# Optimization experiments

Measured on AMD Instinct MI355X. Metric: run time of the kernel, lower is better.

The kernel has to match this reference:

```python
import jax, jax.numpy as jnp
import numpy as np

S, B, D, NH = 4096, 4, 1024, 16


def _unitnorm(v):
    # v / ||v||_2 along last dim (matches torch.norm(v, dim=-1))
    return v / jnp.linalg.norm(v, axis=-1, keepdims=True)


def setup_inputs() -> dict:
    key = jax.random.key(0)
    ks = jax.random.split(key, 9)
    scale = 1.0 / np.sqrt(D)
    inp = {
        "h": jax.random.normal(ks[0], (S, B, D), dtype=jnp.float32),
        "Wq_w": jax.random.normal(ks[1], (D, D), dtype=jnp.float32) * scale,
        "Wq_b": jax.random.normal(ks[2], (D,), dtype=jnp.float32) * scale,
        "Wk_w": jax.random.normal(ks[3], (D, D), dtype=jnp.float32) * scale,
        "Wk_b": jax.random.normal(ks[4], (D,), dtype=jnp.float32) * scale,
        "Wv_w": jax.random.normal(ks[5], (D, D), dtype=jnp.float32) * scale,
        "Wv_b": jax.random.normal(ks[6], (D,), dtype=jnp.float32) * scale,
        "Wo_w": jax.random.normal(ks[7], (D, D), dtype=jnp.float32) * scale,
        "Wo_b": jax.random.normal(ks[8], (D,), dtype=jnp.float32) * scale,
        "nhead": NH,
    }
    return inp


def reference(h, Wq_w, Wq_b, Wk_w, Wk_b, Wv_w, Wv_b, Wo_w, Wo_b, nhead):
    s, b, d = h.shape
    dh = d // nhead

    def proj(W, bias):
        # torch nn.Linear: x @ W.T + b, then split heads -> [S,B,NH,dh]
        return (h @ W.T + bias).reshape(s, b, nhead, dh)

    k = jax.nn.elu(_unitnorm(proj(Wk_w, Wk_b)))  # unitelu
    v = proj(Wv_w, Wv_b)
    q = _unitnorm(proj(Wq_w, Wq_b))  # sigma = unitnorm (default)

    # Linear-attention state: sum of outer products over the whole sequence
    A = jnp.einsum('sbnq,sbnv->bnvq', k, v)  # [B,NH,dh,dh]
    out = jnp.einsum('sbnq,bnvq->sbnv', q, A).reshape(s, b, d)
    out = out @ Wo_w.T + Wo_b
    return out, k, q
```

## Files before the change

### kernel.cpp

```cpp
#include <hip/hip_runtime.h>
#include <hip/hip_bf16.h>
#include <math.h>

#define S_LEN 4096
#define B_SZ  4
#define D_DIM 1024
#define NHEAD 16
#define R_ROWS (S_LEN * B_SZ)

#define AS1 __attribute__((address_space(1)))
#define AS3 __attribute__((address_space(3)))

typedef __bf16 bf16_t;
typedef __attribute__((ext_vector_type(8))) __bf16 bf16x8;
typedef __attribute__((ext_vector_type(4))) __bf16 bf16x4;
typedef __attribute__((ext_vector_type(4))) float  f32x4;

#define MFMA16 __builtin_amdgcn_mfma_f32_16x16x32_bf16

__device__ __forceinline__ void gload16(const bf16_t* g, bf16_t* l) {
  __builtin_amdgcn_global_load_lds((const AS1 unsigned int*)g,
                                   (AS3 unsigned int*)l, 16, 0, 0);
}
__device__ __forceinline__ void hard_barrier() {
  asm volatile("s_barrier" ::: "memory");
}

__global__ void k_cvt(const float* __restrict__ src, bf16_t* __restrict__ dst, int n) {
  int i = (blockIdx.x * 256 + threadIdx.x) * 4;
  if (i >= n) return;
  f32x4 v = *(const f32x4*)(src + i);
  bf16x4 o;
  o[0] = (bf16_t)v[0]; o[1] = (bf16_t)v[1]; o[2] = (bf16_t)v[2]; o[3] = (bf16_t)v[3];
  *(bf16x4*)(dst + i) = o;
}

__device__ __forceinline__ void gemm_core_256(
    const bf16_t* __restrict__ A, const bf16_t* __restrict__ B,
    int row0, int col0,
    bf16_t (&sA)[3][8192], bf16_t (&sB)[3][8192], f32x4 (&acc)[8][4])
{
  const int tid  = threadIdx.x;
  const int wave = tid >> 6, lane = tid & 63;
  const int lr = lane & 15, lg = lane >> 4;
  const int wr = wave >> 2, wn = wave & 3;
  const int grow = tid >> 2;
  const int gch  = (tid & 3) ^ (grow & 3);

  auto stageA = [&](int buf, int k0, int j) {
    gload16(&A[(size_t)(row0 + j * 128 + grow) * D_DIM + k0 + gch * 8],
            &sA[buf][(j * 512 + wave * 64) * 8]);
  };
  auto stageB = [&](int buf, int k0, int j) {
    gload16(&B[(size_t)(col0 + j * 128 + grow) * D_DIM + k0 + gch * 8],
            &sB[buf][(j * 512 + wave * 64) * 8]);
  };

  int aoff[8], boff[4];
  #pragma unroll
  for (int m = 0; m < 8; m++) {
    const int r = wr * 128 + m * 16 + lr;
    aoff[m] = r * 32 + (lg ^ (r & 3)) * 8;
  }
  #pragma unroll
  for (int n = 0; n < 4; n++) {
    const int r = wn * 64 + n * 16 + lr;
    boff[n] = r * 32 + (lg ^ (r & 3)) * 8;
  }

  #pragma unroll
  for (int m = 0; m < 8; m++)
    #pragma unroll
    for (int n = 0; n < 4; n++)
      #pragma unroll
      for (int r = 0; r < 4; r++) acc[m][n][r] = 0.f;

  stageA(0, 0, 0); stageA(0, 0, 1); stageB(0, 0, 0); stageB(0, 0, 1);
  stageA(1, 32, 0); stageA(1, 32, 1); stageB(1, 32, 0); stageB(1, 32, 1);
  asm volatile("s_waitcnt vmcnt(4)" ::: "memory");
  hard_barrier();

  for (int t = 0; t < 32; ++t) {
    const int c  = t % 3;
    const int cn = (t + 2) % 3;
    const int kn = (t + 2) * 32;
    const bool st = (t < 30);

    bf16x8 bfr[4], afr[4];
    #pragma unroll
    for (int n = 0; n < 4; ++n) bfr[n] = *(const bf16x8*)&sB[c][boff[n]];
    #pragma unroll
    for (int m = 0; m < 4; ++m) afr[m] = *(const bf16x8*)&sA[c][aoff[m]];
    if (st) { stageA(cn, kn, 0); stageA(cn, kn, 1); }
    hard_barrier();
    asm volatile("s_waitcnt lgkmcnt(0)" ::: "memory");
    __builtin_amdgcn_sched_barrier(0);
    __builtin_amdgcn_s_setprio(1);
    #pragma unroll
    for (int m = 0; m < 4; ++m)
      #pragma unroll
      for (int n = 0; n < 4; ++n)
        acc[m][n] = MFMA16(afr[m], bfr[n], acc[m][n], 0, 0, 0);
    __builtin_amdgcn_s_setprio(0);
    hard_barrier();

    #pragma unroll
    for (int m = 0; m < 4; ++m) afr[m] = *(const bf16x8*)&sA[c][aoff[m + 4]];
    if (st) { stageB(cn, kn, 0); stageB(cn, kn, 1); }
    hard_barrier();
    asm volatile("s_waitcnt lgkmcnt(0)" ::: "memory");
    __builtin_amdgcn_sched_barrier(0);
    __builtin_amdgcn_s_setprio(1);
    #pragma unroll
    for (int m = 0; m < 4; ++m)
      #pragma unroll
      for (int n = 0; n < 4; ++n)
        acc[m + 4][n] = MFMA16(afr[m], bfr[n], acc[m + 4][n], 0, 0, 0);
    __builtin_amdgcn_s_setprio(0);
    if (t < 30)       asm volatile("s_waitcnt vmcnt(4)" ::: "memory");
    else if (t == 30) asm volatile("s_waitcnt vmcnt(0)" ::: "memory");
    hard_barrier();
  }
}

__global__ __launch_bounds__(512, 2) void k_proj(
    const bf16_t* __restrict__ hB, const bf16_t* __restrict__ Wcat,
    const float* __restrict__ bq, const float* __restrict__ bk, const float* __restrict__ bv,
    bf16_t* __restrict__ outVb, float* __restrict__ outK, float* __restrict__ outQ,
    bf16_t* __restrict__ qBm)
{
  __shared__ bf16_t sA[3][8192];
  __shared__ bf16_t sB[3][8192];

  const int tid  = threadIdx.x;
  const int wave = tid >> 6, lane = tid & 63;
  const int lr = lane & 15, lg = lane >> 4;
  const int wr = wave >> 2, wn = wave & 3;
  const int row0 = blockIdx.x * 256;
  const int by   = blockIdx.y;

  f32x4 acc[8][4];
  gemm_core_256(hB, Wcat, row0, by * 256, sA, sB, acc);

  const int sec = by >> 2;
  const int hc0 = (by & 3) * 256 + wn * 64;
  const float* bias = (sec == 0) ? bq : (sec == 1 ? bk : bv);
  float bvv[4];
  #pragma unroll
  for (int n = 0; n < 4; n++) bvv[n] = bias[hc0 + n * 16 + lr];

  #pragma unroll
  for (int m = 0; m < 8; ++m) {
    #pragma unroll
    for (int r = 0; r < 4; ++r) {
      const int gm = row0 + wr * 128 + m * 16 + lg * 4 + r;
      float v[4];
      float ss = 0.f;
      #pragma unroll
      for (int n = 0; n < 4; n++) {
        v[n] = acc[m][n][r] + bvv[n];
        ss += v[n] * v[n];
      }
      if (sec == 2) {
        #pragma unroll
        for (int n = 0; n < 4; n++)
          outVb[(size_t)gm * D_DIM + hc0 + n * 16 + lr] = (bf16_t)v[n];
      } else {
        #pragma unroll
        for (int msk = 1; msk < 16; msk <<= 1) ss += __shfl_xor(ss, msk);
        const float rs = 1.0f / sqrtf(ss);
        if (sec == 0) {
          const size_t qrow = (size_t)(gm & 3) * S_LEN + (gm >> 2);
          #pragma unroll
          for (int n = 0; n < 4; n++) {
            const float qn = v[n] * rs;
            outQ[(size_t)gm * D_DIM + hc0 + n * 16 + lr] = qn;
            qBm[qrow * D_DIM + hc0 + n * 16 + lr] = (bf16_t)qn;
          }
        } else {
          #pragma unroll
          for (int n = 0; n < 4; n++) {
            float kn = v[n] * rs;
            kn = kn > 0.f ? kn : expm1f(kn);
            outK[(size_t)gm * D_DIM + hc0 + n * 16 + lr] = kn;
          }
        }
      }
    }
  }
}

__global__ __launch_bounds__(256) void k_state(
    const float* __restrict__ Kf, const bf16_t* __restrict__ Vb,
    float* __restrict__ Apart)
{
  const int bn = blockIdx.x;
  const int ch = blockIdx.y;
  const int b = bn >> 4, n = bn & 15;
  const int tid = threadIdx.x;
  const int ti = tid >> 4, tj = tid & 15;

  __shared__ float sV[32][64];
  __shared__ float sK[32][64];

  float acc[4][4];
  #pragma unroll
  for (int i = 0; i < 4; i++)
    #pragma unroll
    for (int j = 0; j < 4; j++) acc[i][j] = 0.f;

  const int rr = tid >> 3, cc = (tid & 7) * 8;
  for (int s0 = ch * 512; s0 < ch * 512 + 512; s0 += 32) {
    const size_t g = (size_t)((s0 + rr) * B_SZ + b) * D_DIM + n * 64 + cc;
    bf16x8 v8 = *(const bf16x8*)&Vb[g];
    #pragma unroll
    for (int e = 0; e < 8; e++) sV[rr][cc + e] = (float)v8[e];
    *(f32x4*)&sK[rr][cc]     = *(const f32x4*)&Kf[g];
    *(f32x4*)&sK[rr][cc + 4] = *(const f32x4*)&Kf[g + 4];
    __syncthreads();
    #pragma unroll
    for (int ss = 0; ss < 32; ss++) {
      f32x4 vv = *(const f32x4*)&sV[ss][ti * 4];
      f32x4 kk = *(const f32x4*)&sK[ss][tj * 4];
      #pragma unroll
      for (int i = 0; i < 4; i++)
        #pragma unroll
        for (int j = 0; j < 4; j++)
          acc[i][j] = fmaf(vv[i], kk[j], acc[i][j]);
    }
    __syncthreads();
  }
  float* ap = Apart + ((size_t)ch * 64 + bn) * 4096;
  #pragma unroll
  for (int i = 0; i < 4; i++)
    #pragma unroll
    for (int j = 0; j < 4; j++)
      ap[(ti * 4 + i) * 64 + tj * 4 + j] = acc[i][j];
}

__global__ __launch_bounds__(256) void k_combine(
    const float* __restrict__ Apart, const bf16_t* __restrict__ WoB,
    bf16_t* __restrict__ Ct)
{
  const int bn = blockIdx.x;
  const int dp = blockIdx.y;
  const int b = bn >> 4, n = bn & 15;
  const int tid = threadIdx.x;
  const int ti = tid >> 4, tj = tid & 15;

  __shared__ float sAm[64][65];
  __shared__ float sW[64][65];

  #pragma unroll
  for (int p = 0; p < 16; p++) {
    const int idx = tid + p * 256;
    float s = 0.f;
    #pragma unroll
    for (int c2 = 0; c2 < 8; c2++)
      s += Apart[((size_t)c2 * 64 + bn) * 4096 + idx];
    sAm[idx >> 6][idx & 63] = s;
  }
  {
    const int r = tid >> 2, cv = (tid & 3) * 16;
    bf16x8 w0 = *(const bf16x8*)&WoB[(size_t)(dp * 64 + r) * D_DIM + n * 64 + cv];
    bf16x8 w1 = *(const bf16x8*)&WoB[(size_t)(dp * 64 + r) * D_DIM + n * 64 + cv + 8];
    #pragma unroll
    for (int e = 0; e < 8; e++) {
      sW[r][cv + e]     = (float)w0[e];
      sW[r][cv + 8 + e] = (float)w1[e];
    }
  }
  __syncthreads();

  float acc[4][4];
  #pragma unroll
  for (int i = 0; i < 4; i++)
    #pragma unroll
    for (int j = 0; j < 4; j++) acc[i][j] = 0.f;

  for (int dv = 0; dv < 64; dv++) {
    float w[4], a[4];
    #pragma unroll
    for (int i = 0; i < 4; i++) w[i] = sW[ti * 4 + i][dv];
    #pragma unroll
    for (int j = 0; j < 4; j++) a[j] = sAm[dv][tj * 4 + j];
    #pragma unroll
    for (int i = 0; i < 4; i++)
      #pragma unroll
      for (int j = 0; j < 4; j++)
        acc[i][j] = fmaf(w[i], a[j], acc[i][j]);
  }
  #pragma unroll
  for (int i = 0; i < 4; i++)
    #pragma unroll
    for (int j = 0; j < 4; j++)
      Ct[((size_t)b * D_DIM + dp * 64 + ti * 4 + i) * D_DIM + n * 64 + tj * 4 + j] =
          (bf16_t)acc[i][j];
}

__global__ __launch_bounds__(512, 2) void k_final(
    const bf16_t* __restrict__ qBm, const bf16_t* __restrict__ Ct,
    const float* __restrict__ bo, float* __restrict__ outO)
{
  __shared__ bf16_t sA[3][8192];
  __shared__ bf16_t sB[3][8192];

  const int tid  = threadIdx.x;
  const int wave = tid >> 6, lane = tid & 63;
  const int lr = lane & 15, lg = lane >> 4;
  const int wr = wave >> 2, wn = wave & 3;
  const int b    = blockIdx.z;
  const int row0 = blockIdx.x * 256;
  const int col0 = blockIdx.y * 256;

  f32x4 acc[8][4];
  gemm_core_256(qBm + (size_t)b * S_LEN * D_DIM, Ct + (size_t)b * D_DIM * D_DIM,
                row0, col0, sA, sB, acc);

  #pragma unroll
  for (int m = 0; m < 8; ++m) {
    #pragma unroll
    for (int r = 0; r < 4; ++r) {
      const int gs = row0 + wr * 128 + m * 16 + lg * 4 + r;
      #pragma unroll
      for (int n = 0; n < 4; n++) {
        const int col = col0 + wn * 64 + n * 16 + lr;
        outO[((size_t)gs * B_SZ + b) * D_DIM + col] = acc[m][n][r] + bo[col];
      }
    }
  }
}

extern "C" void kernel_launch(void* const* d_in, const int* in_sizes, int n_in,
                              void* d_out, int out_size, void* d_ws, size_t ws_size,
                              hipStream_t stream) {
  (void)in_sizes; (void)n_in; (void)out_size; (void)ws_size;
  const float* h  = (const float*)d_in[0];
  const float* Wq = (const float*)d_in[1];
  const float* bq = (const float*)d_in[2];
  const float* Wk = (const float*)d_in[3];
  const float* bk = (const float*)d_in[4];
  const float* Wv = (const float*)d_in[5];
  const float* bv = (const float*)d_in[6];
  const float* Wo = (const float*)d_in[7];
  const float* bo = (const float*)d_in[8];

  float* out0 = (float*)d_out;
  float* outK = out0 + (size_t)R_ROWS * D_DIM;
  float* outQ = outK + (size_t)R_ROWS * D_DIM;
  bf16_t* vB  = (bf16_t*)d_out;

  char* ws = (char*)d_ws;
  bf16_t* hB    = (bf16_t*)ws;
  bf16_t* Ct    = (bf16_t*)ws;
  bf16_t* Wcat  = (bf16_t*)(ws + 33554432);
  bf16_t* WoB   = (bf16_t*)(ws + 33554432 + 6291456);
  float*  Apart = (float*)(ws + 41943040);
  bf16_t* qBm   = (bf16_t*)(ws + 50331648);

  const int nH = R_ROWS * D_DIM;
  const int nW = D_DIM * D_DIM;
  k_cvt<<<nH / 1024, 256, 0, stream>>>(h, hB, nH);
  k_cvt<<<nW / 1024, 256, 0, stream>>>(Wq, Wcat, nW);
  k_cvt<<<nW / 1024, 256, 0, stream>>>(Wk, Wcat + nW, nW);
  k_cvt<<<nW / 1024, 256, 0, stream>>>(Wv, Wcat + 2 * nW, nW);
  k_cvt<<<nW / 1024, 256, 0, stream>>>(Wo, WoB, nW);

  k_proj<<<dim3(R_ROWS / 256, 12), 512, 0, stream>>>(hB, Wcat, bq, bk, bv,
                                                     vB, outK, outQ, qBm);
  k_state<<<dim3(64, 8), 256, 0, stream>>>(outK, vB, Apart);
  k_combine<<<dim3(64, 16), 256, 0, stream>>>(Apart, WoB, Ct);
  k_final<<<dim3(S_LEN / 256, D_DIM / 256, B_SZ), 512, 0, stream>>>(qBm, Ct, bo, out0);
}
```

Before: 265.3 us.

## Restructure GEMM mainloop into 8-phase ping-pong schedule with BK=64 tiles

Result: faster. 254.4 us (-4.1%).

```diff
diff --git a/kernel.cpp b/kernel.cpp
--- a/kernel.cpp
+++ b/kernel.cpp
@@ -22,9 +22,26 @@
   __builtin_amdgcn_global_load_lds((const AS1 unsigned int*)g,
                                    (AS3 unsigned int*)l, 16, 0, 0);
 }
-__device__ __forceinline__ void hard_barrier() {
-  asm volatile("s_barrier" ::: "memory");
-}
+
+#define BAR asm volatile("s_barrier" ::: "memory")
+#define LGKM0 do { asm volatile("s_waitcnt lgkmcnt(0)" ::: "memory"); \
+                   __builtin_amdgcn_sched_barrier(0); } while (0)
+
+#define RD_A(dst, ap, mlo) \
+  _Pragma("unroll") for (int mm = 0; mm < 4; ++mm) \
+    _Pragma("unroll") for (int kx = 0; kx < 2; ++kx) \
+      dst[mm][kx] = *(const bf16x8*)&ap[offA[(mlo) + mm][kx]];
+#define RD_B(dst, bp, nlo) \
+  _Pragma("unroll") for (int nn = 0; nn < 2; ++nn) \
+    _Pragma("unroll") for (int kx = 0; kx < 2; ++kx) \
+      dst[nn][kx] = *(const bf16x8*)&bp[offB[(nlo) + nn][kx]];
+#define QUAD(mb, nb, AF, BF) \
+  do { __builtin_amdgcn_s_setprio(1); \
+  _Pragma("unroll") for (int mm = 0; mm < 4; ++mm) \
+    _Pragma("unroll") for (int nn = 0; nn < 2; ++nn) { \
+      acc[(mb)+mm][(nb)+nn] = MFMA16(AF[mm][0], BF[nn][0], acc[(mb)+mm][(nb)+nn], 0, 0, 0); \
+      acc[(mb)+mm][(nb)+nn] = MFMA16(AF[mm][1], BF[nn][1], acc[(mb)+mm][(nb)+nn], 0, 0, 0); } \
+  __builtin_amdgcn_s_setprio(0); } while (0)
 
 __global__ void k_cvt(const float* __restrict__ src, bf16_t* __restrict__ dst, int n) {
   int i = (blockIdx.x * 256 + threadIdx.x) * 4;
@@ -35,38 +52,50 @@
   *(bf16x4*)(dst + i) = o;
 }
 
-__device__ __forceinline__ void gemm_core_256(
+__device__ __forceinline__ void gemm_core_8ph(
     const bf16_t* __restrict__ A, const bf16_t* __restrict__ B,
     int row0, int col0,
-    bf16_t (&sA)[3][8192], bf16_t (&sB)[3][8192], f32x4 (&acc)[8][4])
+    bf16_t (&sA)[2][2][8192], bf16_t (&sB)[2][2][8192], f32x4 (&acc)[8][4])
 {
   const int tid  = threadIdx.x;
   const int wave = tid >> 6, lane = tid & 63;
   const int lr = lane & 15, lg = lane >> 4;
   const int wr = wave >> 2, wn = wave & 3;
-  const int grow = tid >> 2;
-  const int gch  = (tid & 3) ^ (grow & 3);
-
-  auto stageA = [&](int buf, int k0, int j) {
-    gload16(&A[(size_t)(row0 + j * 128 + grow) * D_DIM + k0 + gch * 8],
-            &sA[buf][(j * 512 + wave * 64) * 8]);
+  const int grow = tid >> 3;
+  const int gsw  = (tid & 7) ^ (grow & 7);
+
+  auto stA = [&](int buf, int half, int k0) {
+    #pragma unroll
+    for (int j = 0; j < 2; ++j)
+      gload16(&A[(size_t)(row0 + half * 128 + j * 64 + grow) * D_DIM + k0 + gsw * 8],
+              &sA[buf][half][(j * 64 + wave * 8) * 64]);
   };
-  auto stageB = [&](int buf, int k0, int j) {
-    gload16(&B[(size_t)(col0 + j * 128 + grow) * D_DIM + k0 + gch * 8],
-            &sB[buf][(j * 512 + wave * 64) * 8]);
+  auto stB = [&](int buf, int half, int k0) {
+    #pragma unroll
+    for (int j = 0; j < 2; ++j)
+      gload16(&B[(size_t)(col0 + half * 128 + j * 64 + grow) * D_DIM + k0 + gsw * 8],
+              &sB[buf][half][(j * 64 + wave * 8) * 64]);
   };
 
-  int aoff[8], boff[4];
-  #pragma unroll
-  for (int m = 0; m < 8; m++) {
-    const int r = wr * 128 + m * 16 + lr;
-    aoff[m] = r * 32 + (lg ^ (r & 3)) * 8;
-  }
-  #pragma unroll
-  for (int n = 0; n < 4; n++) {
-    const int r = wn * 64 + n * 16 + lr;
-    boff[n] = r * 32 + (lg ^ (r & 3)) * 8;
-  }
+  int offA[8][2], offB[4][2];
+  #pragma unroll
+  for (int m = 0; m < 8; ++m) {
+    const int r = m * 16 + lr;
+    #pragma unroll
+    for (int kx = 0; kx < 2; ++kx)
+      offA[m][kx] = r * 64 + (((kx << 2) + lg) ^ (r & 7)) * 8;
+  }
+  #pragma unroll
+  for (int n = 0; n < 4; ++n) {
+    const int r = (wn & 1) * 64 + n * 16 + lr;
+    #pragma unroll
+    for (int kx = 0; kx < 2; ++kx)
+      offB[n][kx] = r * 64 + (((kx << 2) + lg) ^ (r & 7)) * 8;
+  }
+  const bf16_t* a0 = &sA[0][wr][0];
+  const bf16_t* a1 = &sA[1][wr][0];
+  const bf16_t* b0 = &sB[0][wn >> 1][0];
+  const bf16_t* b1 = &sB[1][wn >> 1][0];
 
   #pragma unroll
   for (int m = 0; m < 8; m++)
@@ -75,51 +104,43 @@
       #pragma unroll
       for (int r = 0; r < 4; r++) acc[m][n][r] = 0.f;
 
-  stageA(0, 0, 0); stageA(0, 0, 1); stageB(0, 0, 0); stageB(0, 0, 1);
-  stageA(1, 32, 0); stageA(1, 32, 1); stageB(1, 32, 0); stageB(1, 32, 1);
-  asm volatile("s_waitcnt vmcnt(4)" ::: "memory");
-  hard_barrier();
-
-  for (int t = 0; t < 32; ++t) {
-    const int c  = t % 3;
-    const int cn = (t + 2) % 3;
-    const int kn = (t + 2) * 32;
-    const bool st = (t < 30);
-
-    bf16x8 bfr[4], afr[4];
-    #pragma unroll
-    for (int n = 0; n < 4; ++n) bfr[n] = *(const bf16x8*)&sB[c][boff[n]];
-    #pragma unroll
-    for (int m = 0; m < 4; ++m) afr[m] = *(const bf16x8*)&sA[c][aoff[m]];
-    if (st) { stageA(cn, kn, 0); stageA(cn, kn, 1); }
-    hard_barrier();
-    asm volatile("s_waitcnt lgkmcnt(0)" ::: "memory");
-    __builtin_amdgcn_sched_barrier(0);
-    __builtin_amdgcn_s_setprio(1);
-    #pragma unroll
-    for (int m = 0; m < 4; ++m)
-      #pragma unroll
-      for (int n = 0; n < 4; ++n)
-        acc[m][n] = MFMA16(afr[m], bfr[n], acc[m][n], 0, 0, 0);
-    __builtin_amdgcn_s_setprio(0);
-    hard_barrier();
-
-    #pragma unroll
-    for (int m = 0; m < 4; ++m) afr[m] = *(const bf16x8*)&sA[c][aoff[m + 4]];
-    if (st) { stageB(cn, kn, 0); stageB(cn, kn, 1); }
-    hard_barrier();
-    asm volatile("s_waitcnt lgkmcnt(0)" ::: "memory");
-    __builtin_amdgcn_sched_barrier(0);
-    __builtin_amdgcn_s_setprio(1);
-    #pragma unroll
-    for (int m = 0; m < 4; ++m)
-      #pragma unroll
-      for (int n = 0; n < 4; ++n)
-        acc[m + 4][n] = MFMA16(afr[m], bfr[n], acc[m + 4][n], 0, 0, 0);
-    __builtin_amdgcn_s_setprio(0);
-    if (t < 30)       asm volatile("s_waitcnt vmcnt(4)" ::: "memory");
-    else if (t == 30) asm volatile("s_waitcnt vmcnt(0)" ::: "memory");
-    hard_barrier();
+  stA(0, 0, 0);  stA(0, 1, 0);  stB(0, 0, 0);  stB(0, 1, 0);
+  stA(1, 0, 64); stA(1, 1, 64); stB(1, 0, 64); stB(1, 1, 64);
+  asm volatile("s_waitcnt vmcnt(8)" ::: "memory");
+  BAR;
+
+  bf16x8 af03[4][2], af47[4][2], bf01[2][2], bf23[2][2];
+
+  #pragma unroll 1
+  for (int i = 0; i < 8; ++i) {
+    const bool last = (i == 7);
+    const int kn0 = (i + 1) * 128, kn1 = kn0 + 64;
+
+    RD_A(af03, a0, 0); RD_B(bf01, b0, 0);
+    BAR; LGKM0; QUAD(0, 0, af03, bf01); BAR;
+    RD_A(af47, a0, 4);
+    BAR; LGKM0; QUAD(4, 0, af47, bf01); BAR;
+    RD_B(bf23, b0, 2);
+    if (!last) stA(0, 0, kn0);
+    BAR; LGKM0; QUAD(0, 2, af03, bf23); BAR;
+    if (!last) { stA(0, 1, kn0); stB(0, 0, kn0); }
+    BAR; QUAD(4, 2, af47, bf23);
+    if (!last) asm volatile("s_waitcnt vmcnt(6)" ::: "memory");
+    else       asm volatile("s_waitcnt vmcnt(0)" ::: "memory");
+    BAR;
+
+    RD_A(af03, a1, 0); RD_B(bf01, b1, 0);
+    if (!last) stB(0, 1, kn0);
+    BAR; LGKM0; QUAD(0, 0, af03, bf01); BAR;
+    RD_A(af47, a1, 4);
+    BAR; LGKM0; QUAD(4, 0, af47, bf01); BAR;
+    RD_B(bf23, b1, 2);
+    if (!last) stA(1, 0, kn1);
+    BAR; LGKM0; QUAD(0, 2, af03, bf23); BAR;
+    if (!last) { stA(1, 1, kn1); stB(1, 0, kn1); stB(1, 1, kn1); }
+    BAR; QUAD(4, 2, af47, bf23);
+    if (!last) asm volatile("s_waitcnt vmcnt(8)" ::: "memory");
+    BAR;
   }
 }
 
@@ -129,8 +150,8 @@
     bf16_t* __restrict__ outVb, float* __restrict__ outK, float* __restrict__ outQ,
     bf16_t* __restrict__ qBm)
 {
-  __shared__ bf16_t sA[3][8192];
-  __shared__ bf16_t sB[3][8192];
+  __shared__ bf16_t sA[2][2][8192];
+  __shared__ bf16_t sB[2][2][8192];
 
   const int tid  = threadIdx.x;
   const int wave = tid >> 6, lane = tid & 63;
@@ -140,7 +161,7 @@
   const int by   = blockIdx.y;
 
   f32x4 acc[8][4];
-  gemm_core_256(hB, Wcat, row0, by * 256, sA, sB, acc);
+  gemm_core_8ph(hB, Wcat, row0, by * 256, sA, sB, acc);
 
   const int sec = by >> 2;
   const int hc0 = (by & 3) * 256 + wn * 64;
@@ -302,8 +323,8 @@
     const bf16_t* __restrict__ qBm, const bf16_t* __restrict__ Ct,
     const float* __restrict__ bo, float* __restrict__ outO)
 {
-  __shared__ bf16_t sA[3][8192];
-  __shared__ bf16_t sB[3][8192];
+  __shared__ bf16_t sA[2][2][8192];
+  __shared__ bf16_t sB[2][2][8192];
 
   const int tid  = threadIdx.x;
   const int wave = tid >> 6, lane = tid & 63;
@@ -314,7 +335,7 @@
   const int col0 = blockIdx.y * 256;
 
   f32x4 acc[8][4];
-  gemm_core_256(qBm + (size_t)b * S_LEN * D_DIM, Ct + (size_t)b * D_DIM * D_DIM,
+  gemm_core_8ph(qBm + (size_t)b * S_LEN * D_DIM, Ct + (size_t)b * D_DIM * D_DIM,
                 row0, col0, sA, sB, acc);
 
   #pragma unroll
```

## Shrink GEMM tiles to 128x128 for higher occupancy and fuse weight conversions

Applied to the files above, without the earlier changes.

After: 270.6 us. Within noise of the previous version (+2.0%).

```diff
diff --git a/kernel.cpp b/kernel.cpp
--- a/kernel.cpp
+++ b/kernel.cpp
@@ -22,9 +22,10 @@
   __builtin_amdgcn_global_load_lds((const AS1 unsigned int*)g,
                                    (AS3 unsigned int*)l, 16, 0, 0);
 }
-__device__ __forceinline__ void hard_barrier() {
-  asm volatile("s_barrier" ::: "memory");
-}
+
+#define BAR asm volatile("s_barrier" ::: "memory")
+#define LGKM0 do { asm volatile("s_waitcnt lgkmcnt(0)" ::: "memory"); \
+                   __builtin_amdgcn_sched_barrier(0); } while (0)
 
 __global__ void k_cvt(const float* __restrict__ src, bf16_t* __restrict__ dst, int n) {
   int i = (blockIdx.x * 256 + threadIdx.x) * 4;
@@ -34,126 +35,116 @@
   o[0] = (bf16_t)v[0]; o[1] = (bf16_t)v[1]; o[2] = (bf16_t)v[2]; o[3] = (bf16_t)v[3];
   *(bf16x4*)(dst + i) = o;
 }
-
-__device__ __forceinline__ void gemm_core_256(
+__global__ void k_cvtw(const float* __restrict__ q, const float* __restrict__ k,
+                       const float* __restrict__ v, const float* __restrict__ o,
+                       bf16_t* __restrict__ dst) {
+  const int sec = blockIdx.x >> 10;
+  const int i = ((blockIdx.x & 1023) * 256 + threadIdx.x) * 4;
+  const float* s = (sec == 0) ? q : (sec == 1) ? k : (sec == 2) ? v : o;
+  f32x4 x = *(const f32x4*)(s + i);
+  bf16x4 y;
+  y[0] = (bf16_t)x[0]; y[1] = (bf16_t)x[1]; y[2] = (bf16_t)x[2]; y[3] = (bf16_t)x[3];
+  *(bf16x4*)(dst + (size_t)sec * 1048576 + i) = y;
+}
+
+__device__ __forceinline__ void gemm_core_occ(
     const bf16_t* __restrict__ A, const bf16_t* __restrict__ B,
     int row0, int col0,
-    bf16_t (&sA)[3][8192], bf16_t (&sB)[3][8192], f32x4 (&acc)[8][4])
+    bf16_t (&sA)[3][4096], bf16_t (&sB)[3][4096], f32x4 (&acc)[2][4])
 {
   const int tid  = threadIdx.x;
   const int wave = tid >> 6, lane = tid & 63;
   const int lr = lane & 15, lg = lane >> 4;
-  const int wr = wave >> 2, wn = wave & 3;
-  const int grow = tid >> 2;
-  const int gch  = (tid & 3) ^ (grow & 3);
-
-  auto stageA = [&](int buf, int k0, int j) {
-    gload16(&A[(size_t)(row0 + j * 128 + grow) * D_DIM + k0 + gch * 8],
-            &sA[buf][(j * 512 + wave * 64) * 8]);
+  const int wr = wave >> 1, wn = wave & 1;
+  const int arow = tid >> 2;
+  const int asw  = (tid & 3) ^ ((arow >> 1) & 3);
+
+  auto stA = [&](int buf, int k0) {
+    gload16(&A[(size_t)(row0 + arow) * D_DIM + k0 + asw * 8],
+            &sA[buf][(wave * 64) * 8]);
   };
-  auto stageB = [&](int buf, int k0, int j) {
-    gload16(&B[(size_t)(col0 + j * 128 + grow) * D_DIM + k0 + gch * 8],
-            &sB[buf][(j * 512 + wave * 64) * 8]);
+  auto stB = [&](int buf, int k0) {
+    gload16(&B[(size_t)(col0 + arow) * D_DIM + k0 + asw * 8],
+            &sB[buf][(wave * 64) * 8]);
   };
 
-  int aoff[8], boff[4];
-  #pragma unroll
-  for (int m = 0; m < 8; m++) {
-    const int r = wr * 128 + m * 16 + lr;
-    aoff[m] = r * 32 + (lg ^ (r & 3)) * 8;
-  }
-  #pragma unroll
-  for (int n = 0; n < 4; n++) {
+  int offA[2], offB[4];
+  #pragma unroll
+  for (int m = 0; m < 2; ++m) {
+    const int r = wr * 32 + m * 16 + lr;
+    offA[m] = r * 32 + ((lg ^ ((r >> 1) & 3)) * 8);
+  }
+  #pragma unroll
+  for (int n = 0; n < 4; ++n) {
     const int r = wn * 64 + n * 16 + lr;
-    boff[n] = r * 32 + (lg ^ (r & 3)) * 8;
-  }
-
-  #pragma unroll
-  for (int m = 0; m < 8; m++)
+    offB[n] = r * 32 + ((lg ^ ((r >> 1) & 3)) * 8);
+  }
+
+  #pragma unroll
+  for (int m = 0; m < 2; m++)
     #pragma unroll
     for (int n = 0; n < 4; n++)
       #pragma unroll
       for (int r = 0; r < 4; r++) acc[m][n][r] = 0.f;
 
-  stageA(0, 0, 0); stageA(0, 0, 1); stageB(0, 0, 0); stageB(0, 0, 1);
-  stageA(1, 32, 0); stageA(1, 32, 1); stageB(1, 32, 0); stageB(1, 32, 1);
-  asm volatile("s_waitcnt vmcnt(4)" ::: "memory");
-  hard_barrier();
-
+  stA(0, 0); stB(0, 0); stA(1, 32); stB(1, 32);
+  asm volatile("s_waitcnt vmcnt(2)" ::: "memory");
+  BAR;
+
+  #pragma unroll 1
   for (int t = 0; t < 32; ++t) {
-    const int c  = t % 3;
-    const int cn = (t + 2) % 3;
-    const int kn = (t + 2) * 32;
-    const bool st = (t < 30);
-
-    bf16x8 bfr[4], afr[4];
-    #pragma unroll
-    for (int n = 0; n < 4; ++n) bfr[n] = *(const bf16x8*)&sB[c][boff[n]];
-    #pragma unroll
-    for (int m = 0; m < 4; ++m) afr[m] = *(const bf16x8*)&sA[c][aoff[m]];
-    if (st) { stageA(cn, kn, 0); stageA(cn, kn, 1); }
-    hard_barrier();
-    asm volatile("s_waitcnt lgkmcnt(0)" ::: "memory");
-    __builtin_amdgcn_sched_barrier(0);
+    const int c = t % 3, cn = (t + 2) % 3;
+    bf16x8 af[2], bf[4];
+    #pragma unroll
+    for (int m = 0; m < 2; ++m) af[m] = *(const bf16x8*)&sA[c][offA[m]];
+    #pragma unroll
+    for (int n = 0; n < 4; ++n) bf[n] = *(const bf16x8*)&sB[c][offB[n]];
+    if (t < 30) { stA(cn, (t + 2) * 32); stB(cn, (t + 2) * 32); }
+    LGKM0;
     __builtin_amdgcn_s_setprio(1);
     #pragma unroll
-    for (int m = 0; m < 4; ++m)
+    for (int m = 0; m < 2; ++m)
       #pragma unroll
       for (int n = 0; n < 4; ++n)
-        acc[m][n] = MFMA16(afr[m], bfr[n], acc[m][n], 0, 0, 0);
+        acc[m][n] = MFMA16(af[m], bf[n], acc[m][n], 0, 0, 0);
     __builtin_amdgcn_s_setprio(0);
-    hard_barrier();
-
-    #pragma unroll
-    for (int m = 0; m < 4; ++m) afr[m] = *(const bf16x8*)&sA[c][aoff[m + 4]];
-    if (st) { stageB(cn, kn, 0); stageB(cn, kn, 1); }
-    hard_barrier();
-    asm volatile("s_waitcnt lgkmcnt(0)" ::: "memory");
-    __builtin_amdgcn_sched_barrier(0);
-    __builtin_amdgcn_s_setprio(1);
-    #pragma unroll
-    for (int m = 0; m < 4; ++m)
-      #pragma unroll
-      for (int n = 0; n < 4; ++n)
-        acc[m + 4][n] = MFMA16(afr[m], bfr[n], acc[m + 4][n], 0, 0, 0);
-    __builtin_amdgcn_s_setprio(0);
-    if (t < 30)       asm volatile("s_waitcnt vmcnt(4)" ::: "memory");
+    if (t < 30)       asm volatile("s_waitcnt vmcnt(2)" ::: "memory");
     else if (t == 30) asm volatile("s_waitcnt vmcnt(0)" ::: "memory");
-    hard_barrier();
-  }
-}
-
-__global__ __launch_bounds__(512, 2) void k_proj(
+    BAR;
+  }
+}
+
+__global__ __launch_bounds__(512, 4) void k_proj(
     const bf16_t* __restrict__ hB, const bf16_t* __restrict__ Wcat,
     const float* __restrict__ bq, const float* __restrict__ bk, const float* __restrict__ bv,
     bf16_t* __restrict__ outVb, float* __restrict__ outK, float* __restrict__ outQ,
     bf16_t* __restrict__ qBm)
 {
-  __shared__ bf16_t sA[3][8192];
-  __shared__ bf16_t sB[3][8192];
+  __shared__ bf16_t sA[3][4096];
+  __shared__ bf16_t sB[3][4096];
 
   const int tid  = threadIdx.x;
   const int wave = tid >> 6, lane = tid & 63;
   const int lr = lane & 15, lg = lane >> 4;
-  const int wr = wave >> 2, wn = wave & 3;
-  const int row0 = blockIdx.x * 256;
+  const int wr = wave >> 1, wn = wave & 1;
+  const int row0 = blockIdx.x * 128;
   const int by   = blockIdx.y;
 
-  f32x4 acc[8][4];
-  gemm_core_256(hB, Wcat, row0, by * 256, sA, sB, acc);
-
-  const int sec = by >> 2;
-  const int hc0 = (by & 3) * 256 + wn * 64;
+  f32x4 acc[2][4];
+  gemm_core_occ(hB, Wcat, row0, by * 128, sA, sB, acc);
+
+  const int sec = by >> 3;
+  const int hc0 = (by & 7) * 128 + wn * 64;
   const float* bias = (sec == 0) ? bq : (sec == 1 ? bk : bv);
   float bvv[4];
   #pragma unroll
   for (int n = 0; n < 4; n++) bvv[n] = bias[hc0 + n * 16 + lr];
 
   #pragma unroll
-  for (int m = 0; m < 8; ++m) {
+  for (int m = 0; m < 2; ++m) {
     #pragma unroll
     for (int r = 0; r < 4; ++r) {
-      const int gm = row0 + wr * 128 + m * 16 + lg * 4 + r;
+      const int gm = row0 + wr * 32 + m * 16 + lg * 4 + r;
       float v[4];
       float ss = 0.f;
       #pragma unroll
@@ -298,30 +289,30 @@
           (bf16_t)acc[i][j];
 }
 
-__global__ __launch_bounds__(512, 2) void k_final(
+__global__ __launch_bounds__(512, 4) void k_final(
     const bf16_t* __restrict__ qBm, const bf16_t* __restrict__ Ct,
     const float* __restrict__ bo, float* __restrict__ outO)
 {
-  __shared__ bf16_t sA[3][8192];
-  __shared__ bf16_t sB[3][8192];
+  __shared__ bf16_t sA[3][4096];
+  __shared__ bf16_t sB[3][4096];
 
   const int tid  = threadIdx.x;
   const int wave = tid >> 6, lane = tid & 63;
   const int lr = lane & 15, lg = lane >> 4;
-  const int wr = wave >> 2, wn = wave & 3;
+  const int wr = wave >> 1, wn = wave & 1;
   const int b    = blockIdx.z;
-  const int row0 = blockIdx.x * 256;
-  const int col0 = blockIdx.y * 256;
-
-  f32x4 acc[8][4];
-  gemm_core_256(qBm + (size_t)b * S_LEN * D_DIM, Ct + (size_t)b * D_DIM * D_DIM,
+  const int row0 = blockIdx.x * 128;
+  const int col0 = blockIdx.y * 128;
+
+  f32x4 acc[2][4];
+  gemm_core_occ(qBm + (size_t)b * S_LEN * D_DIM, Ct + (size_t)b * D_DIM * D_DIM,
                 row0, col0, sA, sB, acc);
 
   #pragma unroll
-  for (int m = 0; m < 8; ++m) {
+  for (int m = 0; m < 2; ++m) {
     #pragma unroll
     for (int r = 0; r < 4; ++r) {
-      const int gs = row0 + wr * 128 + m * 16 + lg * 4 + r;
+      const int gs = row0 + wr * 32 + m * 16 + lg * 4 + r;
       #pragma unroll
       for (int n = 0; n < 4; n++) {
         const int col = col0 + wn * 64 + n * 16 + lr;
@@ -359,16 +350,12 @@
   bf16_t* qBm   = (bf16_t*)(ws + 50331648);
 
   const int nH = R_ROWS * D_DIM;
-  const int nW = D_DIM * D_DIM;
   k_cvt<<<nH / 1024, 256, 0, stream>>>(h, hB, nH);
-  k_cvt<<<nW / 1024, 256, 0, stream>>>(Wq, Wcat, nW);
-  k_cvt<<<nW / 1024, 256, 0, stream>>>(Wk, Wcat + nW, nW);
-  k_cvt<<<nW / 1024, 256, 0, stream>>>(Wv, Wcat + 2 * nW, nW);
-  k_cvt<<<nW / 1024, 256, 0, stream>>>(Wo, WoB, nW);
-
-  k_proj<<<dim3(R_ROWS / 256, 12), 512, 0, stream>>>(hB, Wcat, bq, bk, bv,
-                                                     vB, outK, outQ, qBm);
+  k_cvtw<<<4096, 256, 0, stream>>>(Wq, Wk, Wv, Wo, Wcat);
+
+  k_proj<<<dim3(128, 24), 512, 0, stream>>>(hB, Wcat, bq, bk, bv,
+                                            vB, outK, outQ, qBm);
   k_state<<<dim3(64, 8), 256, 0, stream>>>(outK, vB, Apart);
   k_combine<<<dim3(64, 16), 256, 0, stream>>>(Apart, WoB, Ct);
-  k_final<<<dim3(S_LEN / 256, D_DIM / 256, B_SZ), 512, 0, stream>>>(qBm, Ct, bo, out0);
-}
+  k_final<<<dim3(S_LEN / 128, D_DIM / 128, B_SZ), 512, 0, stream>>>(qBm, Ct, bo, out0);
+}
```
